# Optimization experiments

Hardware: AMD Instinct MI355X
Metric: run time of the kernel (lower is better)

## Reference

```python
import jax, jax.numpy as jnp
import numpy as np

B, L, D = 4, 8192, 256          # batch, seq length, embedding dim
H, HD = 8, 32                   # heads, head dim (H*HD == D)
WN, P, S = 9, 4, 1              # window size, padding, stride
EPS = 1e-5


def _layer_norm(x, g, b):
    m = jnp.mean(x, axis=-1, keepdims=True)
    v = jnp.mean(jnp.square(x - m), axis=-1, keepdims=True)
    return (x - m) / jnp.sqrt(v + EPS) * g + b


def setup_inputs() -> dict:
    key = jax.random.key(0)
    ks = jax.random.split(key, 8)
    sc = 0.05
    return {
        "x": jax.random.normal(ks[0], (B, L, D), jnp.float32),
        "W_q": jax.random.normal(ks[1], (D, D), jnp.float32) * sc,
        "W_k": jax.random.normal(ks[2], (D, D), jnp.float32) * sc,
        "W_v": jax.random.normal(ks[3], (D, D), jnp.float32) * sc,
        "W_o": jax.random.normal(ks[4], (D, D), jnp.float32) * sc,
        "pos": jax.random.normal(ks[5], (WN, D), jnp.float32) * sc,
        "W_out": jax.random.normal(ks[6], (D, D), jnp.float32) * sc,
        "b_out": jnp.zeros((D,), jnp.float32),
        "g1": jnp.ones((D,), jnp.float32),
        "b1": jnp.zeros((D,), jnp.float32),
        "g2": jnp.ones((D,), jnp.float32),
        "b2": jnp.zeros((D,), jnp.float32),
    }


def reference(x, W_q, W_k, W_v, W_o, pos, W_out, b_out, g1, b1, g2, b2):
    # input_dim == embedding_dim -> no input projection
    padded = jnp.pad(x, ((0, 0), (P, P), (0, 0)))
    nw = (L + 2 * P - WN) // S + 1  # == L for S=1, WN=2P+1
    idx = jnp.arange(nw)[:, None] * S + jnp.arange(WN)[None, :]  # [nw, WN]
    win = padded[:, idx] + pos  # [B, nw, WN, D]

    def proj(w):  # [B, nw, WN, H, HD]
        return jnp.einsum('bnwd,de->bnwe', win, w).reshape(B, nw, WN, H, HD)

    q, k, v = proj(W_q), proj(W_k), proj(W_v)
    scale = 1.0 / (HD ** 0.5)
    scores = jnp.einsum('bnqhd,bnkhd->bnhqk', q, k) * scale  # [B,nw,H,WN,WN]
    attn = jax.nn.softmax(scores, axis=-1)
    # context, summed over query positions within each window (use_mean=False)
    ctx = jnp.einsum('bnhqk,bnkhd->bnhd', attn, v).reshape(B, nw, D)
    skip = x[:, ::S]  # [B, nw, D]
    attn_res = _layer_norm(skip + ctx @ W_o, g1, b1)
    out = _layer_norm(attn_res @ W_out.T + b_out + attn_res, g2, b2)
    return jax.nn.relu(out)
```

## Files before the change

kernel.cpp:

```cpp
#include <hip/hip_runtime.h>
#include <hip/hip_bf16.h>
#include <math.h>

constexpr int NB   = 4;
constexpr int LL   = 8192;
constexpr int DD   = 256;
constexpr int NH   = 8;
constexpr int HDIM = 32;
constexpr int WNN  = 9;
constexpr int PPAD = 4;

constexpr int CW  = 32;
constexpr int RSN = CW + 8;
constexpr int SST = 260;

typedef __attribute__((ext_vector_type(8))) short bf16x8;
typedef __attribute__((ext_vector_type(4))) float f32x4;

__device__ inline short f2bf(float f) {
  __hip_bfloat16 h = __float2bfloat16(f);
  short s; __builtin_memcpy(&s, &h, 2); return s;
}
__device__ inline float bf2f(short s) {
  unsigned u = ((unsigned)(unsigned short)s) << 16;
  float f; __builtin_memcpy(&f, &u, 4); return f;
}

__global__ __launch_bounds__(256) void conv_x(const float* __restrict__ x, short* __restrict__ XB) {
  size_t i = ((size_t)blockIdx.x * 256 + threadIdx.x) * 4;
  float4 v = *(const float4*)(x + i);
  short4 o; o.x = f2bf(v.x); o.y = f2bf(v.y); o.z = f2bf(v.z); o.w = f2bf(v.w);
  *(short4*)(XB + i) = o;
}

__global__ __launch_bounds__(256) void prep_w(
    const float* __restrict__ Wq, const float* __restrict__ Wk, const float* __restrict__ Wv,
    const float* __restrict__ Wo, const float* __restrict__ Wout,
    short* __restrict__ WqT, short* __restrict__ WkT, short* __restrict__ WvT,
    short* __restrict__ WoT, short* __restrict__ WoutB) {
  const int t = threadIdx.x, b = blockIdx.x;
  if (b < 4) {
    const float* W = (b == 0) ? Wq : (b == 1) ? Wk : (b == 2) ? Wv : Wo;
    short* T = (b == 0) ? WqT : (b == 1) ? WkT : (b == 2) ? WvT : WoT;
    for (int k = 0; k < 256; k += 4) {
      short4 o;
      o.x = f2bf(W[(size_t)(k + 0) * 256 + t]);
      o.y = f2bf(W[(size_t)(k + 1) * 256 + t]);
      o.z = f2bf(W[(size_t)(k + 2) * 256 + t]);
      o.w = f2bf(W[(size_t)(k + 3) * 256 + t]);
      *(short4*)&T[(size_t)t * 256 + k] = o;
    }
  } else {
    for (int i = t; i < 16384; i += 256) {
      float4 v = *(const float4*)(Wout + (size_t)i * 4);
      short4 o; o.x = f2bf(v.x); o.y = f2bf(v.y); o.z = f2bf(v.z); o.w = f2bf(v.w);
      *(short4*)(WoutB + (size_t)i * 4) = o;
    }
  }
}

__global__ __launch_bounds__(256) void pos_proj(
    const float* __restrict__ pos,
    const float* __restrict__ Wq, const float* __restrict__ Wk, const float* __restrict__ Wv,
    short* __restrict__ PQb, short* __restrict__ PKb, short* __restrict__ PVb) {
  __shared__ float ps[256];
  const int t = threadIdx.x, wrow = blockIdx.x, wh = blockIdx.y;
  const float* W = (wh == 0) ? Wq : (wh == 1) ? Wk : Wv;
  short* P = (wh == 0) ? PQb : (wh == 1) ? PKb : PVb;
  ps[t] = pos[wrow * 256 + t];
  __syncthreads();
  float a = 0.f;
  for (int d = 0; d < 256; ++d) a += ps[d] * W[(size_t)d * 256 + t];
  P[wrow * 256 + t] = f2bf(a);
}

__global__ __launch_bounds__(256) void qkv_mfma(
    const short* __restrict__ XB,
    const short* __restrict__ WT0, const short* __restrict__ WT1, const short* __restrict__ WT2,
    short* __restrict__ O0, short* __restrict__ O1, short* __restrict__ O2) {
  const int t = threadIdx.x, w = t >> 6, lane = t & 63, q = lane >> 4, m = lane & 15;
  const size_t row0 = (size_t)blockIdx.x * 64;
  const short* WT = (blockIdx.y == 0) ? WT0 : (blockIdx.y == 1) ? WT1 : WT2;
  short* O = (blockIdx.y == 0) ? O0 : (blockIdx.y == 1) ? O1 : O2;

  f32x4 acc[4][4];
#pragma unroll
  for (int i = 0; i < 4; ++i)
#pragma unroll
    for (int j = 0; j < 4; ++j) acc[i][j] = (f32x4){0.f, 0.f, 0.f, 0.f};

  const short* abase = XB + (row0 + m) * (size_t)256 + q * 8;
  const short* bbase = WT + (size_t)(w * 64 + m) * 256 + q * 8;
  bf16x8 a[4], b[4];
#pragma unroll
  for (int i = 0; i < 4; ++i) a[i] = *(const bf16x8*)(abase + (size_t)i * 4096);
#pragma unroll
  for (int j = 0; j < 4; ++j) b[j] = *(const bf16x8*)(bbase + (size_t)j * 4096);
#pragma unroll
  for (int kk = 0; kk < 8; ++kk) {
    bf16x8 an[4], bn[4];
    if (kk < 7) {
#pragma unroll
      for (int i = 0; i < 4; ++i) an[i] = *(const bf16x8*)(abase + (size_t)i * 4096 + (kk + 1) * 32);
#pragma unroll
      for (int j = 0; j < 4; ++j) bn[j] = *(const bf16x8*)(bbase + (size_t)j * 4096 + (kk + 1) * 32);
    }
#pragma unroll
    for (int i = 0; i < 4; ++i)
#pragma unroll
      for (int j = 0; j < 4; ++j)
        acc[i][j] = __builtin_amdgcn_mfma_f32_16x16x32_bf16(a[i], b[j], acc[i][j], 0, 0, 0);
    if (kk < 7) {
#pragma unroll
      for (int i = 0; i < 4; ++i) a[i] = an[i];
#pragma unroll
      for (int j = 0; j < 4; ++j) b[j] = bn[j];
    }
  }
#pragma unroll
  for (int i = 0; i < 4; ++i)
#pragma unroll
    for (int j = 0; j < 4; ++j)
#pragma unroll
      for (int r = 0; r < 4; ++r) {
        size_t row = row0 + i * 16 + q * 4 + r;
        int col = w * 64 + j * 16 + m;
        O[row * 256 + col] = f2bf(acc[i][j][r]);
      }
}

__global__ __launch_bounds__(256, 2) void attn_kernel(
    const short* __restrict__ XQb, const short* __restrict__ XKb, const short* __restrict__ XVb,
    const short* __restrict__ PQb, const short* __restrict__ PKb, const short* __restrict__ PVb,
    short* __restrict__ CTXB) {
  __shared__ short sq[RSN * SST];
  __shared__ short sk[RSN * SST];
  __shared__ short sv[RSN * SST];
  __shared__ short pq[WNN * SST];
  __shared__ short pk[WNN * SST];
  __shared__ short pv[WNN * SST];

  const int t = threadIdx.x;
  const int nblk = LL / CW;
  const int b = blockIdx.x / nblk;
  const int n0 = (blockIdx.x % nblk) * CW;
  const size_t base = (size_t)b * LL * DD;

#pragma unroll
  for (int i = 0; i < RSN * 64 / 256; ++i) {
    int idx = t + i * 256;
    int r = idx >> 6, c4 = (idx & 63) * 4;
    int j = n0 - PPAD + r;
    short4 vq = {0, 0, 0, 0}, vk = vq, vv = vq;
    if (j >= 0 && j < LL) {
      size_t off = base + (size_t)j * DD + c4;
      vq = *(const short4*)(XQb + off);
      vk = *(const short4*)(XKb + off);
      vv = *(const short4*)(XVb + off);
    }
    *(short4*)&sq[r * SST + c4] = vq;
    *(short4*)&sk[r * SST + c4] = vk;
    *(short4*)&sv[r * SST + c4] = vv;
  }
#pragma unroll
  for (int i = 0; i < 3; ++i) {
    int idx = t + i * 256;
    if (idx < WNN * 64) {
      int r = idx >> 6, c4 = (idx & 63) * 4;
      *(short4*)&pq[r * SST + c4] = *(const short4*)(PQb + r * DD + c4);
      *(short4*)&pk[r * SST + c4] = *(const short4*)(PKb + r * DD + c4);
      *(short4*)&pv[r * SST + c4] = *(const short4*)(PVb + r * DD + c4);
    }
  }
  __syncthreads();

  const int n = t >> 3;
  const int h = t & 7;
  const int hoff = h * HDIM;

  float sc[WNN][WNN];
#pragma unroll
  for (int qi = 0; qi < WNN; ++qi)
#pragma unroll
    for (int ki = 0; ki < WNN; ++ki) sc[qi][ki] = 0.f;

#pragma unroll
  for (int c = 0; c < 8; ++c) {
    float qv[WNN][4], kv[WNN][4];
#pragma unroll
    for (int r = 0; r < WNN; ++r) {
      short4 xa = *(const short4*)&sq[(n + r) * SST + hoff + c * 4];
      short4 pa = *(const short4*)&pq[r * SST + hoff + c * 4];
      qv[r][0] = bf2f(xa.x) + bf2f(pa.x);
      qv[r][1] = bf2f(xa.y) + bf2f(pa.y);
      qv[r][2] = bf2f(xa.z) + bf2f(pa.z);
      qv[r][3] = bf2f(xa.w) + bf2f(pa.w);
      short4 xb = *(const short4*)&sk[(n + r) * SST + hoff + c * 4];
      short4 pb = *(const short4*)&pk[r * SST + hoff + c * 4];
      kv[r][0] = bf2f(xb.x) + bf2f(pb.x);
      kv[r][1] = bf2f(xb.y) + bf2f(pb.y);
      kv[r][2] = bf2f(xb.z) + bf2f(pb.z);
      kv[r][3] = bf2f(xb.w) + bf2f(pb.w);
    }
#pragma unroll
    for (int qi = 0; qi < WNN; ++qi)
#pragma unroll
      for (int ki = 0; ki < WNN; ++ki)
        sc[qi][ki] += qv[qi][0] * kv[ki][0] + qv[qi][1] * kv[ki][1] +
                      qv[qi][2] * kv[ki][2] + qv[qi][3] * kv[ki][3];
  }

  float cs[WNN];
#pragma unroll
  for (int ki = 0; ki < WNN; ++ki) cs[ki] = 0.f;
  const float scale = 0.17677669529663687f;
#pragma unroll
  for (int qi = 0; qi < WNN; ++qi) {
    float mx = sc[qi][0];
#pragma unroll
    for (int ki = 1; ki < WNN; ++ki) mx = fmaxf(mx, sc[qi][ki]);
    float e[WNN], sum = 0.f;
#pragma unroll
    for (int ki = 0; ki < WNN; ++ki) { e[ki] = __expf((sc[qi][ki] - mx) * scale); sum += e[ki]; }
    float inv = 1.f / sum;
#pragma unroll
    for (int ki = 0; ki < WNN; ++ki) cs[ki] += e[ki] * inv;
  }

#pragma unroll
  for (int c = 0; c < 8; ++c) {
    float o0 = 0.f, o1 = 0.f, o2 = 0.f, o3 = 0.f;
#pragma unroll
    for (int ki = 0; ki < WNN; ++ki) {
      short4 xv4 = *(const short4*)&sv[(n + ki) * SST + hoff + c * 4];
      short4 pv4 = *(const short4*)&pv[ki * SST + hoff + c * 4];
      float wt = cs[ki];
      o0 += wt * (bf2f(xv4.x) + bf2f(pv4.x));
      o1 += wt * (bf2f(xv4.y) + bf2f(pv4.y));
      o2 += wt * (bf2f(xv4.z) + bf2f(pv4.z));
      o3 += wt * (bf2f(xv4.w) + bf2f(pv4.w));
    }
    short4 os; os.x = f2bf(o0); os.y = f2bf(o1); os.z = f2bf(o2); os.w = f2bf(o3);
    *(short4*)(CTXB + base + (size_t)(n0 + n) * DD + hoff + c * 4) = os;
  }
}


__global__ __launch_bounds__(256) void out_mfma(
    const short* __restrict__ CTXB, const float* __restrict__ X,
    const short* __restrict__ WoT, const short* __restrict__ WoutB,
    const float* __restrict__ bo,
    const float* __restrict__ g1, const float* __restrict__ b1,
    const float* __restrict__ g2, const float* __restrict__ b2,
    float* __restrict__ out) {
  __shared__ short ar[64 * 264];
  __shared__ float ws1[64][4], ws2[64][4];
  __shared__ float msh[64], rsh[64];
  __shared__ float g1s[256], b1s[256], g2s[256], b2s[256], bos[256];
  const int t = threadIdx.x, w = t >> 6, lane = t & 63, q = lane >> 4, m = lane & 15;
  const size_t row0 = (size_t)blockIdx.x * 64;
  g1s[t] = g1[t]; b1s[t] = b1[t]; g2s[t] = g2[t]; b2s[t] = b2[t]; bos[t] = bo[t];

  f32x4 acc[4][4];
#pragma unroll
  for (int i = 0; i < 4; ++i)
#pragma unroll
    for (int j = 0; j < 4; ++j) acc[i][j] = (f32x4){0.f, 0.f, 0.f, 0.f};

  const short* abase = CTXB + (row0 + m) * (size_t)256 + q * 8;
  const short* bbase = WoT + (size_t)(w * 64 + m) * 256 + q * 8;
  {
    bf16x8 a[4], b[4];
#pragma unroll
    for (int i = 0; i < 4; ++i) a[i] = *(const bf16x8*)(abase + (size_t)i * 4096);
#pragma unroll
    for (int j = 0; j < 4; ++j) b[j] = *(const bf16x8*)(bbase + (size_t)j * 4096);
#pragma unroll
    for (int kk = 0; kk < 8; ++kk) {
      bf16x8 an[4], bn[4];
      if (kk < 7) {
#pragma unroll
        for (int i = 0; i < 4; ++i) an[i] = *(const bf16x8*)(abase + (size_t)i * 4096 + (kk + 1) * 32);
#pragma unroll
        for (int j = 0; j < 4; ++j) bn[j] = *(const bf16x8*)(bbase + (size_t)j * 4096 + (kk + 1) * 32);
      }
#pragma unroll
      for (int i = 0; i < 4; ++i)
#pragma unroll
        for (int j = 0; j < 4; ++j)
          acc[i][j] = __builtin_amdgcn_mfma_f32_16x16x32_bf16(a[i], b[j], acc[i][j], 0, 0, 0);
      if (kk < 7) {
#pragma unroll
        for (int i = 0; i < 4; ++i) a[i] = an[i];
#pragma unroll
        for (int j = 0; j < 4; ++j) b[j] = bn[j];
      }
    }
  }

  float s1v[4][4], s2v[4][4];
#pragma unroll
  for (int i = 0; i < 4; ++i)
#pragma unroll
    for (int r = 0; r < 4; ++r) {
      float a0 = 0.f, b0 = 0.f;
#pragma unroll
      for (int j = 0; j < 4; ++j) {
        float v = acc[i][j][r] + X[(row0 + i * 16 + q * 4 + r) * 256 + w * 64 + j * 16 + m];
        acc[i][j][r] = v; a0 += v; b0 += v * v;
      }
      s1v[i][r] = a0; s2v[i][r] = b0;
    }
#pragma unroll
  for (int i = 0; i < 4; ++i)
#pragma unroll
    for (int r = 0; r < 4; ++r)
#pragma unroll
      for (int msk = 1; msk < 16; msk <<= 1) {
        s1v[i][r] += __shfl_xor(s1v[i][r], msk, 64);
        s2v[i][r] += __shfl_xor(s2v[i][r], msk, 64);
      }
  if (m == 0) {
#pragma unroll
    for (int i = 0; i < 4; ++i)
#pragma unroll
      for (int r = 0; r < 4; ++r) {
        ws1[i * 16 + q * 4 + r][w] = s1v[i][r];
        ws2[i * 16 + q * 4 + r][w] = s2v[i][r];
      }
  }
  __syncthreads();
  if (t < 64) {
    float a0 = 0.f, b0 = 0.f;
#pragma unroll
    for (int ww = 0; ww < 4; ++ww) { a0 += ws1[t][ww]; b0 += ws2[t][ww]; }
    float mean = a0 * (1.f / 256.f);
    float var = b0 * (1.f / 256.f) - mean * mean;
    msh[t] = mean; rsh[t] = rsqrtf(var + 1e-5f);
  }
  __syncthreads();

#pragma unroll
  for (int i = 0; i < 4; ++i)
#pragma unroll
    for (int r = 0; r < 4; ++r) {
      int row = i * 16 + q * 4 + r;
      float mean = msh[row], rst = rsh[row];
#pragma unroll
      for (int j = 0; j < 4; ++j) {
        int col = w * 64 + j * 16 + m;
        float v = (acc[i][j][r] - mean) * rst * g1s[col] + b1s[col];
        ar[row * 264 + col] = f2bf(v);
      }
    }
  __syncthreads();

#pragma unroll
  for (int i = 0; i < 4; ++i)
#pragma unroll
    for (int j = 0; j < 4; ++j) acc[i][j] = (f32x4){0.f, 0.f, 0.f, 0.f};
  const short* b2base = WoutB + (size_t)(w * 64 + m) * 256 + q * 8;
  {
    bf16x8 b[4];
#pragma unroll
    for (int j = 0; j < 4; ++j) b[j] = *(const bf16x8*)(b2base + (size_t)j * 4096);
#pragma unroll
    for (int kk = 0; kk < 8; ++kk) {
      bf16x8 bn[4];
      if (kk < 7) {
#pragma unroll
        for (int j = 0; j < 4; ++j) bn[j] = *(const bf16x8*)(b2base + (size_t)j * 4096 + (kk + 1) * 32);
      }
      bf16x8 a[4];
#pragma unroll
      for (int i = 0; i < 4; ++i) a[i] = *(const bf16x8*)&ar[(i * 16 + m) * 264 + kk * 32 + q * 8];
#pragma unroll
      for (int i = 0; i < 4; ++i)
#pragma unroll
        for (int j = 0; j < 4; ++j)
          acc[i][j] = __builtin_amdgcn_mfma_f32_16x16x32_bf16(a[i], b[j], acc[i][j], 0, 0, 0);
      if (kk < 7) {
#pragma unroll
        for (int j = 0; j < 4; ++j) b[j] = bn[j];
      }
    }
  }

#pragma unroll
  for (int i = 0; i < 4; ++i)
#pragma unroll
    for (int r = 0; r < 4; ++r) {
      int row = i * 16 + q * 4 + r;
      float a0 = 0.f, b0 = 0.f;
#pragma unroll
      for (int j = 0; j < 4; ++j) {
        int col = w * 64 + j * 16 + m;
        float v = acc[i][j][r] + bos[col] + bf2f(ar[row * 264 + col]);
        acc[i][j][r] = v; a0 += v; b0 += v * v;
      }
      s1v[i][r] = a0; s2v[i][r] = b0;
    }
#pragma unroll
  for (int i = 0; i < 4; ++i)
#pragma unroll
    for (int r = 0; r < 4; ++r)
#pragma unroll
      for (int msk = 1; msk < 16; msk <<= 1) {
        s1v[i][r] += __shfl_xor(s1v[i][r], msk, 64);
        s2v[i][r] += __shfl_xor(s2v[i][r], msk, 64);
      }
  if (m == 0) {
#pragma unroll
    for (int i = 0; i < 4; ++i)
#pragma unroll
      for (int r = 0; r < 4; ++r) {
        ws1[i * 16 + q * 4 + r][w] = s1v[i][r];
        ws2[i * 16 + q * 4 + r][w] = s2v[i][r];
      }
  }
  __syncthreads();
  if (t < 64) {
    float a0 = 0.f, b0 = 0.f;
#pragma unroll
    for (int ww = 0; ww < 4; ++ww) { a0 += ws1[t][ww]; b0 += ws2[t][ww]; }
    float mean = a0 * (1.f / 256.f);
    float var = b0 * (1.f / 256.f) - mean * mean;
    msh[t] = mean; rsh[t] = rsqrtf(var + 1e-5f);
  }
  __syncthreads();

#pragma unroll
  for (int i = 0; i < 4; ++i)
#pragma unroll
    for (int r = 0; r < 4; ++r) {
      int row = i * 16 + q * 4 + r;
      float mean = msh[row], rst = rsh[row];
#pragma unroll
      for (int j = 0; j < 4; ++j) {
        int col = w * 64 + j * 16 + m;
        float v = (acc[i][j][r] - mean) * rst * g2s[col] + b2s[col];
        out[(row0 + row) * 256 + col] = fmaxf(v, 0.f);
      }
    }
}

extern "C" void kernel_launch(void* const* d_in, const int* in_sizes, int n_in,
                              void* d_out, int out_size, void* d_ws, size_t ws_size,
                              hipStream_t stream) {
  const float* x    = (const float*)d_in[0];
  const float* Wq   = (const float*)d_in[1];
  const float* Wk   = (const float*)d_in[2];
  const float* Wv   = (const float*)d_in[3];
  const float* Wo   = (const float*)d_in[4];
  const float* pos  = (const float*)d_in[5];
  const float* Wout = (const float*)d_in[6];
  const float* bo   = (const float*)d_in[7];
  const float* g1   = (const float*)d_in[8];
  const float* b1   = (const float*)d_in[9];
  const float* g2   = (const float*)d_in[10];
  const float* b2   = (const float*)d_in[11];
  float* out = (float*)d_out;

  const size_t nel = (size_t)NB * LL * DD;
  char* wsb = (char*)d_ws;
  short* XB   = (short*)wsb; wsb += nel * 2;
  short* XQb  = (short*)wsb; wsb += nel * 2;
  short* XKb  = (short*)wsb; wsb += nel * 2;
  short* XVb  = (short*)wsb; wsb += nel * 2;
  short* CTXB = (short*)wsb; wsb += nel * 2;
  short* WqT   = (short*)wsb; wsb += 65536 * 2;
  short* WkT   = (short*)wsb; wsb += 65536 * 2;
  short* WvT   = (short*)wsb; wsb += 65536 * 2;
  short* WoT   = (short*)wsb; wsb += 65536 * 2;
  short* WoutB = (short*)wsb; wsb += 65536 * 2;
  short* PQb = (short*)wsb; wsb += WNN * DD * 2;
  short* PKb = (short*)wsb; wsb += WNN * DD * 2;
  short* PVb = (short*)wsb; wsb += WNN * DD * 2;

  conv_x<<<(unsigned)(nel / 4 / 256), 256, 0, stream>>>(x, XB);
  prep_w<<<5, 256, 0, stream>>>(Wq, Wk, Wv, Wo, Wout, WqT, WkT, WvT, WoT, WoutB);
  pos_proj<<<dim3(WNN, 3), 256, 0, stream>>>(pos, Wq, Wk, Wv, PQb, PKb, PVb);
  qkv_mfma<<<dim3((unsigned)(NB * LL / 64), 3), 256, 0, stream>>>(XB, WqT, WkT, WvT, XQb, XKb, XVb);
  attn_kernel<<<NB * (LL / CW), 256, 0, stream>>>(XQb, XKb, XVb, PQb, PKb, PVb, CTXB);
  out_mfma<<<(unsigned)(NB * LL / 64), 256, 0, stream>>>(CTXB, x, WoT, WoutB, bo, g1, b1, g2, b2, out);
}
```

Measured before the change: 273.0 us.

## Decompose windowed attention scores into shared token-pair and positional terms

The scores are expanded as (xq+pq)·(xk+pk) = xq·xk + xq·pk + pq·xk + pq·pk. Each term is computed once per token or token pair and stored in shared tables, rather than recomputed for every window. Because the token-pair dot products are shared across overlapping windows, the redundant score FLOPs drop, and one shared buffer is reused for K and then V. The cost is extra synchronisation phases, more LDS for the tables, bf16 rounding of the cross terms, and removal of the two-blocks-per-CU occupancy hint.

```diff
diff --git a/kernel.cpp b/kernel.cpp
--- a/kernel.cpp
+++ b/kernel.cpp
@@ -13,6 +13,7 @@
 constexpr int CW  = 32;
 constexpr int RSN = CW + 8;
 constexpr int SST = 260;
+constexpr int PST = 260;
 
 typedef __attribute__((ext_vector_type(8))) short bf16x8;
 typedef __attribute__((ext_vector_type(4))) float f32x4;
@@ -129,16 +130,18 @@
       }
 }
 
-__global__ __launch_bounds__(256, 2) void attn_kernel(
+__global__ __launch_bounds__(256) void attn_kernel(
     const short* __restrict__ XQb, const short* __restrict__ XKb, const short* __restrict__ XVb,
     const short* __restrict__ PQb, const short* __restrict__ PKb, const short* __restrict__ PVb,
     short* __restrict__ CTXB) {
-  __shared__ short sq[RSN * SST];
-  __shared__ short sk[RSN * SST];
-  __shared__ short sv[RSN * SST];
-  __shared__ short pq[WNN * SST];
-  __shared__ short pk[WNN * SST];
-  __shared__ short pv[WNN * SST];
+  __shared__ short skv[RSN * SST];
+  __shared__ short pq[WNN * PST];
+  __shared__ short pk[WNN * PST];
+  __shared__ short pv[WNN * PST];
+  __shared__ float Dt[NH * RSN * 18];
+  __shared__ short Et[NH * RSN * 10];
+  __shared__ short Ft[NH * 10 * RSN];
+  __shared__ float Gt[NH * WNN * 12];
 
   const int t = threadIdx.x;
   const int nblk = LL / CW;
@@ -151,89 +154,149 @@
     int idx = t + i * 256;
     int r = idx >> 6, c4 = (idx & 63) * 4;
     int j = n0 - PPAD + r;
-    short4 vq = {0, 0, 0, 0}, vk = vq, vv = vq;
-    if (j >= 0 && j < LL) {
-      size_t off = base + (size_t)j * DD + c4;
-      vq = *(const short4*)(XQb + off);
-      vk = *(const short4*)(XKb + off);
-      vv = *(const short4*)(XVb + off);
-    }
-    *(short4*)&sq[r * SST + c4] = vq;
-    *(short4*)&sk[r * SST + c4] = vk;
-    *(short4*)&sv[r * SST + c4] = vv;
+    short4 v = {0, 0, 0, 0};
+    if (j >= 0 && j < LL) v = *(const short4*)(XKb + base + (size_t)j * DD + c4);
+    *(short4*)&skv[r * SST + c4] = v;
   }
 #pragma unroll
   for (int i = 0; i < 3; ++i) {
     int idx = t + i * 256;
     if (idx < WNN * 64) {
       int r = idx >> 6, c4 = (idx & 63) * 4;
-      *(short4*)&pq[r * SST + c4] = *(const short4*)(PQb + r * DD + c4);
-      *(short4*)&pk[r * SST + c4] = *(const short4*)(PKb + r * DD + c4);
-      *(short4*)&pv[r * SST + c4] = *(const short4*)(PVb + r * DD + c4);
-    }
-  }
-  __syncthreads();
-
-  const int n = t >> 3;
-  const int h = t & 7;
-  const int hoff = h * HDIM;
-
-  float sc[WNN][WNN];
-#pragma unroll
-  for (int qi = 0; qi < WNN; ++qi)
-#pragma unroll
-    for (int ki = 0; ki < WNN; ++ki) sc[qi][ki] = 0.f;
-
-#pragma unroll
-  for (int c = 0; c < 8; ++c) {
-    float qv[WNN][4], kv[WNN][4];
-#pragma unroll
-    for (int r = 0; r < WNN; ++r) {
-      short4 xa = *(const short4*)&sq[(n + r) * SST + hoff + c * 4];
-      short4 pa = *(const short4*)&pq[r * SST + hoff + c * 4];
-      qv[r][0] = bf2f(xa.x) + bf2f(pa.x);
-      qv[r][1] = bf2f(xa.y) + bf2f(pa.y);
-      qv[r][2] = bf2f(xa.z) + bf2f(pa.z);
-      qv[r][3] = bf2f(xa.w) + bf2f(pa.w);
-      short4 xb = *(const short4*)&sk[(n + r) * SST + hoff + c * 4];
-      short4 pb = *(const short4*)&pk[r * SST + hoff + c * 4];
-      kv[r][0] = bf2f(xb.x) + bf2f(pb.x);
-      kv[r][1] = bf2f(xb.y) + bf2f(pb.y);
-      kv[r][2] = bf2f(xb.z) + bf2f(pb.z);
-      kv[r][3] = bf2f(xb.w) + bf2f(pb.w);
-    }
-#pragma unroll
-    for (int qi = 0; qi < WNN; ++qi)
-#pragma unroll
-      for (int ki = 0; ki < WNN; ++ki)
-        sc[qi][ki] += qv[qi][0] * kv[ki][0] + qv[qi][1] * kv[ki][1] +
-                      qv[qi][2] * kv[ki][2] + qv[qi][3] * kv[ki][3];
-  }
-
+      *(short4*)&pq[r * PST + c4] = *(const short4*)(PQb + r * DD + c4);
+      *(short4*)&pk[r * PST + c4] = *(const short4*)(PKb + r * DD + c4);
+      *(short4*)&pv[r * PST + c4] = *(const short4*)(PVb + r * DD + c4);
+    }
+  }
+  __syncthreads();
+
+  for (int u = t; u < RSN * NH; u += 256) {
+    const int r = u >> 3, h = u & 7;
+    const int hoff = h * HDIM;
+    float xqf[32];
+    {
+      int j = n0 - PPAD + r;
+      if (j >= 0 && j < LL) {
+        const short* p = XQb + base + (size_t)j * DD + hoff;
+#pragma unroll
+        for (int c = 0; c < 8; ++c) {
+          short4 v = *(const short4*)(p + c * 4);
+          xqf[c * 4 + 0] = bf2f(v.x); xqf[c * 4 + 1] = bf2f(v.y);
+          xqf[c * 4 + 2] = bf2f(v.z); xqf[c * 4 + 3] = bf2f(v.w);
+        }
+      } else {
+#pragma unroll
+        for (int i = 0; i < 32; ++i) xqf[i] = 0.f;
+      }
+    }
+    for (int dd = 0; dd < 17; ++dd) {
+      int jr = r + dd - 8;
+      float acc = 0.f;
+      if (jr >= 0 && jr < RSN) {
+        const short* kp = &skv[jr * SST + hoff];
+#pragma unroll
+        for (int c = 0; c < 8; ++c) {
+          short4 kv = *(const short4*)(kp + c * 4);
+          acc += xqf[c * 4] * bf2f(kv.x) + xqf[c * 4 + 1] * bf2f(kv.y) +
+                 xqf[c * 4 + 2] * bf2f(kv.z) + xqf[c * 4 + 3] * bf2f(kv.w);
+        }
+      }
+      Dt[h * (RSN * 18) + r * 18 + dd] = acc;
+    }
+#pragma unroll
+    for (int k = 0; k < WNN; ++k) {
+      const short* kp = &pk[k * PST + hoff];
+      float acc = 0.f;
+#pragma unroll
+      for (int c = 0; c < 8; ++c) {
+        short4 kv = *(const short4*)(kp + c * 4);
+        acc += xqf[c * 4] * bf2f(kv.x) + xqf[c * 4 + 1] * bf2f(kv.y) +
+               xqf[c * 4 + 2] * bf2f(kv.z) + xqf[c * 4 + 3] * bf2f(kv.w);
+      }
+      Et[h * (RSN * 10) + r * 10 + k] = f2bf(acc);
+    }
+    float xkf[32];
+    {
+      const short* p = &skv[r * SST + hoff];
+#pragma unroll
+      for (int c = 0; c < 8; ++c) {
+        short4 v = *(const short4*)(p + c * 4);
+        xkf[c * 4 + 0] = bf2f(v.x); xkf[c * 4 + 1] = bf2f(v.y);
+        xkf[c * 4 + 2] = bf2f(v.z); xkf[c * 4 + 3] = bf2f(v.w);
+      }
+    }
+#pragma unroll
+    for (int qq = 0; qq < WNN; ++qq) {
+      const short* qp = &pq[qq * PST + hoff];
+      float acc = 0.f;
+#pragma unroll
+      for (int c = 0; c < 8; ++c) {
+        short4 qv = *(const short4*)(qp + c * 4);
+        acc += xkf[c * 4] * bf2f(qv.x) + xkf[c * 4 + 1] * bf2f(qv.y) +
+               xkf[c * 4 + 2] * bf2f(qv.z) + xkf[c * 4 + 3] * bf2f(qv.w);
+      }
+      Ft[h * (10 * RSN) + qq * RSN + r] = f2bf(acc);
+    }
+  }
+  for (int u = t; u < NH * WNN * WNN; u += 256) {
+    int h = u / 81, rem = u % 81, qq = rem / 9, k = rem % 9;
+    const short* qp = &pq[qq * PST + h * HDIM];
+    const short* kp = &pk[k * PST + h * HDIM];
+    float acc = 0.f;
+#pragma unroll
+    for (int c = 0; c < 8; ++c) {
+      short4 qv = *(const short4*)(qp + c * 4);
+      short4 kv = *(const short4*)(kp + c * 4);
+      acc += bf2f(qv.x) * bf2f(kv.x) + bf2f(qv.y) * bf2f(kv.y) +
+             bf2f(qv.z) * bf2f(kv.z) + bf2f(qv.w) * bf2f(kv.w);
+    }
+    Gt[h * 108 + qq * 12 + k] = acc;
+  }
+  __syncthreads();
+
+#pragma unroll
+  for (int i = 0; i < RSN * 64 / 256; ++i) {
+    int idx = t + i * 256;
+    int r = idx >> 6, c4 = (idx & 63) * 4;
+    int j = n0 - PPAD + r;
+    short4 v = {0, 0, 0, 0};
+    if (j >= 0 && j < LL) v = *(const short4*)(XVb + base + (size_t)j * DD + c4);
+    *(short4*)&skv[r * SST + c4] = v;
+  }
+  __syncthreads();
+
+  const int n = t >> 3, h = t & 7, hoff = h * HDIM;
   float cs[WNN];
 #pragma unroll
-  for (int ki = 0; ki < WNN; ++ki) cs[ki] = 0.f;
+  for (int k = 0; k < WNN; ++k) cs[k] = 0.f;
   const float scale = 0.17677669529663687f;
 #pragma unroll
-  for (int qi = 0; qi < WNN; ++qi) {
-    float mx = sc[qi][0];
-#pragma unroll
-    for (int ki = 1; ki < WNN; ++ki) mx = fmaxf(mx, sc[qi][ki]);
-    float e[WNN], sum = 0.f;
-#pragma unroll
-    for (int ki = 0; ki < WNN; ++ki) { e[ki] = __expf((sc[qi][ki] - mx) * scale); sum += e[ki]; }
+  for (int q = 0; q < WNN; ++q) {
+    const int lr = n + q;
+    const float* Dp = &Dt[h * (RSN * 18) + lr * 18];
+    const short* Ep = &Et[h * (RSN * 10) + lr * 10];
+    const short* Fp = &Ft[h * (10 * RSN) + q * RSN + n];
+    const float* Gp = &Gt[h * 108 + q * 12];
+    float s_[9]; float mx = -1e30f;
+#pragma unroll
+    for (int k = 0; k < 9; ++k) {
+      s_[k] = Dp[8 + k - q] + bf2f(Ep[k]) + bf2f(Fp[k]) + Gp[k];
+      mx = fmaxf(mx, s_[k]);
+    }
+    float e_[9], sum = 0.f;
+#pragma unroll
+    for (int k = 0; k < 9; ++k) { e_[k] = __expf((s_[k] - mx) * scale); sum += e_[k]; }
     float inv = 1.f / sum;
 #pragma unroll
-    for (int ki = 0; ki < WNN; ++ki) cs[ki] += e[ki] * inv;
-  }
-
+    for (int k = 0; k < 9; ++k) cs[k] += e_[k] * inv;
+  }
 #pragma unroll
   for (int c = 0; c < 8; ++c) {
     float o0 = 0.f, o1 = 0.f, o2 = 0.f, o3 = 0.f;
 #pragma unroll
     for (int ki = 0; ki < WNN; ++ki) {
-      short4 xv4 = *(const short4*)&sv[(n + ki) * SST + hoff + c * 4];
-      short4 pv4 = *(const short4*)&pv[ki * SST + hoff + c * 4];
+      short4 xv4 = *(const short4*)&skv[(n + ki) * SST + hoff + c * 4];
+      short4 pv4 = *(const short4*)&pv[ki * PST + hoff + c * 4];
       float wt = cs[ki];
       o0 += wt * (bf2f(xv4.x) + bf2f(pv4.x));
       o1 += wt * (bf2f(xv4.y) + bf2f(pv4.y));
@@ -244,7 +307,6 @@
     *(short4*)(CTXB + base + (size_t)(n0 + n) * DD + hoff + c * 4) = os;
   }
 }
-
 
 __global__ __launch_bounds__(256) void out_mfma(
     const short* __restrict__ CTXB, const float* __restrict__ X,
```

New measurement: 336.2 us. 23.2% more time.

## Fuse x conversion into QKV GMEM kernel and merge weight prep kernels

Applied to the files above, without the earlier changes.

Drops the separate fp32-to-bf16 conversion pass over x. The QKV kernel now loads fp32 x tiles, converts them into shared memory, and computes all three Q/K/V projections from that one tile, so x is read once instead of three times and the bf16 copy buffer is no longer written. Weight transpose, Wout conversion and the positional projection are merged into one 71-block launch, using shared-memory tiled transposes and more parallel blocks than the old 5-block serial version. In exchange each QKV block holds more accumulators, the row tile shrinks to 32, and weights are read straight from global memory without prefetching, which may reduce occupancy or latency hiding.

```diff
diff --git a/kernel.cpp b/kernel.cpp
--- a/kernel.cpp
+++ b/kernel.cpp
@@ -26,107 +26,111 @@
   float f; __builtin_memcpy(&f, &u, 4); return f;
 }
 
-__global__ __launch_bounds__(256) void conv_x(const float* __restrict__ x, short* __restrict__ XB) {
-  size_t i = ((size_t)blockIdx.x * 256 + threadIdx.x) * 4;
-  float4 v = *(const float4*)(x + i);
-  short4 o; o.x = f2bf(v.x); o.y = f2bf(v.y); o.z = f2bf(v.z); o.w = f2bf(v.w);
-  *(short4*)(XB + i) = o;
-}
-
-__global__ __launch_bounds__(256) void prep_w(
+__global__ __launch_bounds__(256) void prep_all(
     const float* __restrict__ Wq, const float* __restrict__ Wk, const float* __restrict__ Wv,
-    const float* __restrict__ Wo, const float* __restrict__ Wout,
+    const float* __restrict__ Wo, const float* __restrict__ Wout, const float* __restrict__ pos,
     short* __restrict__ WqT, short* __restrict__ WkT, short* __restrict__ WvT,
-    short* __restrict__ WoT, short* __restrict__ WoutB) {
+    short* __restrict__ WoT, short* __restrict__ WoutB,
+    short* __restrict__ PQb, short* __restrict__ PKb, short* __restrict__ PVb) {
+  __shared__ float sm[64 * 65];
   const int t = threadIdx.x, b = blockIdx.x;
-  if (b < 4) {
-    const float* W = (b == 0) ? Wq : (b == 1) ? Wk : (b == 2) ? Wv : Wo;
-    short* T = (b == 0) ? WqT : (b == 1) ? WkT : (b == 2) ? WvT : WoT;
-    for (int k = 0; k < 256; k += 4) {
-      short4 o;
-      o.x = f2bf(W[(size_t)(k + 0) * 256 + t]);
-      o.y = f2bf(W[(size_t)(k + 1) * 256 + t]);
-      o.z = f2bf(W[(size_t)(k + 2) * 256 + t]);
-      o.w = f2bf(W[(size_t)(k + 3) * 256 + t]);
-      *(short4*)&T[(size_t)t * 256 + k] = o;
+  if (b < 64) {
+    const int wi = b >> 4, tile = b & 15;
+    const int r0 = (tile >> 2) * 64, c0 = (tile & 3) * 64;
+    const float* W = (wi == 0) ? Wq : (wi == 1) ? Wk : (wi == 2) ? Wv : Wo;
+    short* T = (wi == 0) ? WqT : (wi == 1) ? WkT : (wi == 2) ? WvT : WoT;
+    const int tr = t >> 6, tc = t & 63;
+#pragma unroll
+    for (int i = 0; i < 16; ++i) {
+      int r = tr + i * 4;
+      sm[r * 65 + tc] = W[(size_t)(r0 + r) * 256 + c0 + tc];
+    }
+    __syncthreads();
+#pragma unroll
+    for (int i = 0; i < 16; ++i) {
+      int cj = tr + i * 4;
+      T[(size_t)(c0 + cj) * 256 + r0 + tc] = f2bf(sm[tc * 65 + cj]);
+    }
+  } else if (b < 68) {
+    const int idx = b - 64;
+    for (int i = t; i < 4096; i += 256) {
+      float4 v = *(const float4*)(Wout + ((size_t)idx * 4096 + i) * 4);
+      short4 o; o.x = f2bf(v.x); o.y = f2bf(v.y); o.z = f2bf(v.z); o.w = f2bf(v.w);
+      *(short4*)(WoutB + ((size_t)idx * 4096 + i) * 4) = o;
     }
   } else {
-    for (int i = t; i < 16384; i += 256) {
-      float4 v = *(const float4*)(Wout + (size_t)i * 4);
-      short4 o; o.x = f2bf(v.x); o.y = f2bf(v.y); o.z = f2bf(v.z); o.w = f2bf(v.w);
-      *(short4*)(WoutB + (size_t)i * 4) = o;
-    }
-  }
-}
-
-__global__ __launch_bounds__(256) void pos_proj(
-    const float* __restrict__ pos,
-    const float* __restrict__ Wq, const float* __restrict__ Wk, const float* __restrict__ Wv,
-    short* __restrict__ PQb, short* __restrict__ PKb, short* __restrict__ PVb) {
-  __shared__ float ps[256];
-  const int t = threadIdx.x, wrow = blockIdx.x, wh = blockIdx.y;
-  const float* W = (wh == 0) ? Wq : (wh == 1) ? Wk : Wv;
-  short* P = (wh == 0) ? PQb : (wh == 1) ? PKb : PVb;
-  ps[t] = pos[wrow * 256 + t];
-  __syncthreads();
-  float a = 0.f;
-  for (int d = 0; d < 256; ++d) a += ps[d] * W[(size_t)d * 256 + t];
-  P[wrow * 256 + t] = f2bf(a);
-}
-
-__global__ __launch_bounds__(256) void qkv_mfma(
-    const short* __restrict__ XB,
+    const int wh = b - 68;
+    const float* W = (wh == 0) ? Wq : (wh == 1) ? Wk : Wv;
+    short* P = (wh == 0) ? PQb : (wh == 1) ? PKb : PVb;
+    for (int i = t; i < WNN * 256; i += 256) sm[i] = pos[i];
+    __syncthreads();
+    float a[WNN];
+#pragma unroll
+    for (int w = 0; w < WNN; ++w) a[w] = 0.f;
+    for (int d = 0; d < 256; ++d) {
+      float wv = W[(size_t)d * 256 + t];
+#pragma unroll
+      for (int w = 0; w < WNN; ++w) a[w] += sm[w * 256 + d] * wv;
+    }
+#pragma unroll
+    for (int w = 0; w < WNN; ++w) P[w * 256 + t] = f2bf(a[w]);
+  }
+}
+
+__global__ __launch_bounds__(256) void qkv_fused(
+    const float* __restrict__ x,
     const short* __restrict__ WT0, const short* __restrict__ WT1, const short* __restrict__ WT2,
     short* __restrict__ O0, short* __restrict__ O1, short* __restrict__ O2) {
+  __shared__ short xs[32 * 264];
   const int t = threadIdx.x, w = t >> 6, lane = t & 63, q = lane >> 4, m = lane & 15;
-  const size_t row0 = (size_t)blockIdx.x * 64;
-  const short* WT = (blockIdx.y == 0) ? WT0 : (blockIdx.y == 1) ? WT1 : WT2;
-  short* O = (blockIdx.y == 0) ? O0 : (blockIdx.y == 1) ? O1 : O2;
-
-  f32x4 acc[4][4];
-#pragma unroll
-  for (int i = 0; i < 4; ++i)
-#pragma unroll
-    for (int j = 0; j < 4; ++j) acc[i][j] = (f32x4){0.f, 0.f, 0.f, 0.f};
-
-  const short* abase = XB + (row0 + m) * (size_t)256 + q * 8;
-  const short* bbase = WT + (size_t)(w * 64 + m) * 256 + q * 8;
-  bf16x8 a[4], b[4];
-#pragma unroll
-  for (int i = 0; i < 4; ++i) a[i] = *(const bf16x8*)(abase + (size_t)i * 4096);
-#pragma unroll
-  for (int j = 0; j < 4; ++j) b[j] = *(const bf16x8*)(bbase + (size_t)j * 4096);
+  const size_t row0 = (size_t)blockIdx.x * 32;
+
+#pragma unroll
+  for (int i = 0; i < 8; ++i) {
+    int idx = t + i * 256;
+    int r = idx >> 6, c4 = (idx & 63) * 4;
+    float4 v = *(const float4*)(x + (row0 + r) * 256 + c4);
+    short4 o; o.x = f2bf(v.x); o.y = f2bf(v.y); o.z = f2bf(v.z); o.w = f2bf(v.w);
+    *(short4*)&xs[r * 264 + c4] = o;
+  }
+  __syncthreads();
+
+  f32x4 acc[3][2][4];
+#pragma unroll
+  for (int bu = 0; bu < 3; ++bu)
+#pragma unroll
+    for (int i = 0; i < 2; ++i)
+#pragma unroll
+      for (int j = 0; j < 4; ++j) acc[bu][i][j] = (f32x4){0.f, 0.f, 0.f, 0.f};
+
 #pragma unroll
   for (int kk = 0; kk < 8; ++kk) {
-    bf16x8 an[4], bn[4];
-    if (kk < 7) {
-#pragma unroll
-      for (int i = 0; i < 4; ++i) an[i] = *(const bf16x8*)(abase + (size_t)i * 4096 + (kk + 1) * 32);
-#pragma unroll
-      for (int j = 0; j < 4; ++j) bn[j] = *(const bf16x8*)(bbase + (size_t)j * 4096 + (kk + 1) * 32);
-    }
-#pragma unroll
-    for (int i = 0; i < 4; ++i)
+    bf16x8 a[2];
+#pragma unroll
+    for (int i = 0; i < 2; ++i) a[i] = *(const bf16x8*)&xs[(i * 16 + m) * 264 + kk * 32 + q * 8];
+#pragma unroll
+    for (int bu = 0; bu < 3; ++bu) {
+      const short* WT = (bu == 0) ? WT0 : (bu == 1) ? WT1 : WT2;
+#pragma unroll
+      for (int j = 0; j < 4; ++j) {
+        bf16x8 bb = *(const bf16x8*)(WT + (size_t)(w * 64 + j * 16 + m) * 256 + kk * 32 + q * 8);
+#pragma unroll
+        for (int i = 0; i < 2; ++i)
+          acc[bu][i][j] = __builtin_amdgcn_mfma_f32_16x16x32_bf16(a[i], bb, acc[bu][i][j], 0, 0, 0);
+      }
+    }
+  }
+#pragma unroll
+  for (int bu = 0; bu < 3; ++bu) {
+    short* O = (bu == 0) ? O0 : (bu == 1) ? O1 : O2;
+#pragma unroll
+    for (int i = 0; i < 2; ++i)
 #pragma unroll
       for (int j = 0; j < 4; ++j)
-        acc[i][j] = __builtin_amdgcn_mfma_f32_16x16x32_bf16(a[i], b[j], acc[i][j], 0, 0, 0);
-    if (kk < 7) {
-#pragma unroll
-      for (int i = 0; i < 4; ++i) a[i] = an[i];
-#pragma unroll
-      for (int j = 0; j < 4; ++j) b[j] = bn[j];
-    }
-  }
-#pragma unroll
-  for (int i = 0; i < 4; ++i)
-#pragma unroll
-    for (int j = 0; j < 4; ++j)
-#pragma unroll
-      for (int r = 0; r < 4; ++r) {
-        size_t row = row0 + i * 16 + q * 4 + r;
-        int col = w * 64 + j * 16 + m;
-        O[row * 256 + col] = f2bf(acc[i][j][r]);
-      }
+#pragma unroll
+        for (int r = 0; r < 4; ++r)
+          O[(row0 + i * 16 + q * 4 + r) * 256 + w * 64 + j * 16 + m] = f2bf(acc[bu][i][j][r]);
+  }
 }
 
 __global__ __launch_bounds__(256, 2) void attn_kernel(
@@ -219,7 +223,8 @@
     float mx = sc[qi][0];
 #pragma unroll
     for (int ki = 1; ki < WNN; ++ki) mx = fmaxf(mx, sc[qi][ki]);
-    float e[WNN], sum = 0.f;
+    float sum = 0.f;
+    float e[WNN];
 #pragma unroll
     for (int ki = 0; ki < WNN; ++ki) { e[ki] = __expf((sc[qi][ki] - mx) * scale); sum += e[ki]; }
     float inv = 1.f / sum;
@@ -244,7 +249,6 @@
     *(short4*)(CTXB + base + (size_t)(n0 + n) * DD + hoff + c * 4) = os;
   }
 }
-
 
 __global__ __launch_bounds__(256) void out_mfma(
     const short* __restrict__ CTXB, const float* __restrict__ X,
@@ -463,7 +467,6 @@
 
   const size_t nel = (size_t)NB * LL * DD;
   char* wsb = (char*)d_ws;
-  short* XB   = (short*)wsb; wsb += nel * 2;
   short* XQb  = (short*)wsb; wsb += nel * 2;
   short* XKb  = (short*)wsb; wsb += nel * 2;
   short* XVb  = (short*)wsb; wsb += nel * 2;
@@ -477,10 +480,9 @@
   short* PKb = (short*)wsb; wsb += WNN * DD * 2;
   short* PVb = (short*)wsb; wsb += WNN * DD * 2;
 
-  conv_x<<<(unsigned)(nel / 4 / 256), 256, 0, stream>>>(x, XB);
-  prep_w<<<5, 256, 0, stream>>>(Wq, Wk, Wv, Wo, Wout, WqT, WkT, WvT, WoT, WoutB);
-  pos_proj<<<dim3(WNN, 3), 256, 0, stream>>>(pos, Wq, Wk, Wv, PQb, PKb, PVb);
-  qkv_mfma<<<dim3((unsigned)(NB * LL / 64), 3), 256, 0, stream>>>(XB, WqT, WkT, WvT, XQb, XKb, XVb);
+  prep_all<<<71, 256, 0, stream>>>(Wq, Wk, Wv, Wo, Wout, pos,
+                                   WqT, WkT, WvT, WoT, WoutB, PQb, PKb, PVb);
+  qkv_fused<<<(unsigned)(NB * LL / 32), 256, 0, stream>>>(x, WqT, WkT, WvT, XQb, XKb, XVb);
   attn_kernel<<<NB * (LL / CW), 256, 0, stream>>>(XQb, XKb, XVb, PQb, PKb, PVb, CTXB);
   out_mfma<<<(unsigned)(NB * LL / 64), 256, 0, stream>>>(CTXB, x, WoT, WoutB, bo, g1, b1, g2, b2, out);
 }
```

Result: no change. 273.1 us (+0.0%).
